# Optimization experiments

Hardware: AMD Instinct MI355X
Metric: run time of the kernel (lower is better)

## Reference

```python
import jax, jax.numpy as jnp
import numpy as np

D_MODEL = 1024
NUM_HEADS = 16
D_K = D_MODEL // NUM_HEADS
BATCH = 2
SEQ = 2048
SCALE = 1.0 / np.sqrt(D_K)


def _rope_tables(seq_len, d_k):
    # theta_i = 10000^(-2i/d_k), i in [0, d_k/2)
    theta = 10000.0 ** (-2.0 * jnp.arange(d_k // 2, dtype=jnp.float32) / d_k)
    angles = jnp.arange(seq_len, dtype=jnp.float32)[:, None] * theta[None, :]  # [S, d_k/2]
    return jnp.sin(angles), jnp.cos(angles)


def _apply_rope(x, sin, cos):
    # x: [B, H, S, d_k]; interleaved rotation over even/odd feature pairs
    xe = x[..., 0::2]
    xo = x[..., 1::2]
    re = xe * cos - xo * sin
    ro = xe * sin + xo * cos
    return jnp.stack([re, ro], axis=-1).reshape(x.shape)


def setup_inputs() -> dict:
    key = jax.random.key(0)
    ks = jax.random.split(key, 12)
    s = 0.02
    inp = {
        'q_input': jax.random.normal(ks[0], (BATCH, SEQ, D_MODEL), jnp.float32),
        'k_input': jax.random.normal(ks[1], (BATCH, SEQ, D_MODEL), jnp.float32),
        'v_input': jax.random.normal(ks[2], (BATCH, SEQ, D_MODEL), jnp.float32),
        'mask': jnp.tril(jnp.ones((SEQ, SEQ), jnp.int32)),  # causal 2D mask
        'W_q': jax.random.normal(ks[3], (D_MODEL, D_MODEL), jnp.float32) * s,
        'b_q': jnp.zeros((D_MODEL,), jnp.float32),
        'W_k': jax.random.normal(ks[4], (D_MODEL, D_MODEL), jnp.float32) * s,
        'b_k': jnp.zeros((D_MODEL,), jnp.float32),
        'W_v': jax.random.normal(ks[5], (D_MODEL, D_MODEL), jnp.float32) * s,
        'b_v': jnp.zeros((D_MODEL,), jnp.float32),
        'W_o': jax.random.normal(ks[6], (D_MODEL, D_MODEL), jnp.float32) * s,
        'b_o': jnp.zeros((D_MODEL,), jnp.float32),
    }
    return inp


def reference(q_input, k_input, v_input, mask, W_q, b_q, W_k, b_k, W_v, b_v, W_o, b_o):
    B, S, _ = q_input.shape
    # projections -> [B, H, S, d_k]
    def proj(x, W, b):
        y = x @ W + b
        return y.reshape(B, -1, NUM_HEADS, D_K).transpose(0, 2, 1, 3)
    q = proj(q_input, W_q, b_q)
    k = proj(k_input, W_k, b_k)
    v = proj(v_input, W_v, b_v)

    sin, cos = _rope_tables(S, D_K)
    q = _apply_rope(q, sin, cos)
    k = _apply_rope(k, sin, cos)

    scores = jnp.einsum('bhqd,bhkd->bhqk', q, k) * SCALE
    scores = jnp.where(mask[None, None, :, :] == 0, jnp.float32(-1e9), scores)
    attn = jax.nn.softmax(scores, axis=-1)  # dropout is identity (p=0 / eval)
    ctx = jnp.einsum('bhqk,bhkd->bhqd', attn, v)
    ctx = ctx.transpose(0, 2, 1, 3).reshape(B, S, D_MODEL)
    return ctx @ W_o + b_o
```

## Files before the change

kernel.cpp:

```cpp
#include <hip/hip_runtime.h>

typedef unsigned short u16;
typedef unsigned int u32;
typedef __attribute__((ext_vector_type(8))) short short8;
typedef __attribute__((ext_vector_type(4))) float f32x4;
typedef __attribute__((ext_vector_type(16))) float f32x16;

#define DEV static __device__ __forceinline__

DEV u16 f2bf(float x) {
  union { float f; u32 u; } v; v.f = x;
  u32 r = v.u + 0x7fffu + ((v.u >> 16) & 1u);
  return (u16)(r >> 16);
}
DEV float bf2f(u16 x) {
  union { u32 u; float f; } v; v.u = ((u32)x) << 16;
  return v.f;
}
DEV u32 cvtpk(float lo, float hi) {
  u32 r;
  asm("v_cvt_pk_bf16_f32 %0, %1, %2" : "=v"(r) : "v"(lo), "v"(hi));
  return r;
}
DEV void swap32(u32& a, u32& b) {
  asm("v_permlane32_swap_b32 %0, %1" : "+v"(a), "+v"(b));
}
DEV float ex2(float x) {
  float r;
  asm("v_exp_f32 %0, %1" : "=v"(r) : "v"(x));
  return r;
}

DEV void gload_lds16(const void* g, void* l) {
  __builtin_amdgcn_global_load_lds(
      (__attribute__((address_space(1))) u32*)((void*)g),
      (__attribute__((address_space(3))) u32*)l, 16, 0, 0);
}

DEV void mfma_bf16(f32x4& d, short8 a, short8 b) {
  asm("v_mfma_f32_16x16x32_bf16 %0, %1, %2, %0" : "+v"(d) : "v"(a), "v"(b));
}
DEV void mfma32(f32x16& d, short8 a, short8 b) {
  asm("v_mfma_f32_32x32x16_bf16 %0, %1, %2, %0" : "+v"(d) : "v"(a), "v"(b));
}

__global__ __launch_bounds__(256) void k_prep(const float* __restrict__ x0, const float* __restrict__ x1,
                                              const float* __restrict__ x2, u16* __restrict__ o0,
                                              u16* __restrict__ o1, u16* __restrict__ o2,
                                              const float* __restrict__ W0, const float* __restrict__ W1,
                                              const float* __restrict__ W2, const float* __restrict__ W3,
                                              u16* __restrict__ T0, u16* __restrict__ T1,
                                              u16* __restrict__ T2, u16* __restrict__ T3,
                                              float2* __restrict__ tab) {
  int bid = blockIdx.x;
  int t = threadIdx.x;
  if (bid < 6144) {
    int z = bid >> 11;
    const float* in = (z == 0) ? x0 : (z == 1) ? x1 : x2;
    u16* out = (z == 0) ? o0 : (z == 1) ? o1 : o2;
    int i = (bid & 2047) * 256 + t;
    const float4* p = (const float4*)in;
    float4 a = p[i * 2], b = p[i * 2 + 1];
    uint4 o;
    o.x = cvtpk(a.x, a.y); o.y = cvtpk(a.z, a.w);
    o.z = cvtpk(b.x, b.y); o.w = cvtpk(b.z, b.w);
    ((uint4*)out)[i] = o;
  } else if (bid < 7168) {
    int q = bid - 6144;
    int z = q >> 8;
    const float* W = (z == 0) ? W0 : (z == 1) ? W1 : (z == 2) ? W2 : W3;
    u16* Wt = (z == 0) ? T0 : (z == 1) ? T1 : (z == 2) ? T2 : T3;
    __shared__ u16 tile[64][65];
    int k0 = ((q >> 4) & 15) * 64, n0 = (q & 15) * 64;
    int rr = t >> 4, cc = (t & 15) * 4;
#pragma unroll
    for (int i = 0; i < 4; ++i) {
      int r = rr + i * 16;
      float4 v = *(const float4*)&W[(size_t)(k0 + r) * 1024 + n0 + cc];
      tile[r][cc + 0] = f2bf(v.x); tile[r][cc + 1] = f2bf(v.y);
      tile[r][cc + 2] = f2bf(v.z); tile[r][cc + 3] = f2bf(v.w);
    }
    __syncthreads();
#pragma unroll
    for (int i = 0; i < 4; ++i) {
      int n = rr + i * 16;
      u16 a0 = tile[cc + 0][n], a1 = tile[cc + 1][n], a2 = tile[cc + 2][n], a3 = tile[cc + 3][n];
      uint2 pk;
      pk.x = (u32)a0 | ((u32)a1 << 16);
      pk.y = (u32)a2 | ((u32)a3 << 16);
      *(uint2*)&Wt[(size_t)(n0 + n) * 1024 + k0 + cc] = pk;
    }
  } else {
    int idx = (bid - 7168) * 256 + t;
    int s = idx >> 5, dp = idx & 31;
    float theta = exp2f((float)dp * (-2.0f / 64.0f) * 13.287712379549449f);
    float ang = (float)s * theta;
    float sn, cs;
    sincosf(ang, &sn, &cs);
    tab[idx] = make_float2(cs, sn);
  }
}

#define GEMM_BODY(A_, Bt_)                                                                       \
  __shared__ __align__(16) char sA[16384];                                                       \
  __shared__ __align__(16) char sB[16384];                                                       \
  int tid = threadIdx.x, lane = tid & 63, w = tid >> 6;                                          \
  int l15 = lane & 15, lg = lane >> 4;                                                           \
  int bm = blockIdx.x * 128, bn = blockIdx.y * 128;                                              \
  int wm = (w >> 1) * 64, wn = (w & 1) * 64;                                                     \
  f32x4 acc[4][4];                                                                               \
  _Pragma("unroll") for (int i = 0; i < 4; ++i)                                                  \
      _Pragma("unroll") for (int j = 0; j < 4; ++j) acc[i][j] = (f32x4){0.f, 0.f, 0.f, 0.f};     \
  for (int kt = 0; kt < 16; ++kt) {                                                              \
    _Pragma("unroll") for (int p = 0; p < 4; ++p) {                                              \
      int idx = p * 256 + tid;                                                                   \
      int row = idx >> 3;                                                                        \
      int c8 = (idx & 7) ^ (row & 7);                                                            \
      gload_lds16(A_ + (size_t)(bm + row) * 1024 + kt * 64 + c8 * 8, sA + p * 4096 + w * 1024);  \
      gload_lds16(Bt_ + (size_t)(bn + row) * 1024 + kt * 64 + c8 * 8, sB + p * 4096 + w * 1024); \
    }                                                                                            \
    __syncthreads();                                                                             \
    short8 af[4][2], bf[4][2];                                                                   \
    _Pragma("unroll") for (int i = 0; i < 4; ++i) _Pragma("unroll") for (int s = 0; s < 2; ++s) { \
      int cs = ((s * 4 + lg) ^ (l15 & 7)) * 16;                                                  \
      af[i][s] = *(const short8*)(sA + (wm + i * 16 + l15) * 128 + cs);                          \
      bf[i][s] = *(const short8*)(sB + (wn + i * 16 + l15) * 128 + cs);                          \
    }                                                                                            \
    _Pragma("unroll") for (int s = 0; s < 2; ++s)                                                \
        _Pragma("unroll") for (int i = 0; i < 4; ++i)                                            \
            _Pragma("unroll") for (int j = 0; j < 4; ++j) mfma_bf16(acc[i][j], af[i][s], bf[j][s]); \
    __syncthreads();                                                                             \
  }

template <int MODE>
__global__ __launch_bounds__(256) void k_gemm(const u16* __restrict__ A, const u16* __restrict__ Bt,
                                              const float* __restrict__ bias, void* __restrict__ dst) {
  GEMM_BODY(A, Bt)
  float bv[4];
#pragma unroll
  for (int j = 0; j < 4; ++j) bv[j] = bias[bn + wn + j * 16 + l15];
#pragma unroll
  for (int i = 0; i < 4; ++i) {
#pragma unroll
    for (int j = 0; j < 4; ++j) {
#pragma unroll
      for (int r = 0; r < 4; ++r) {
        int m = bm + wm + i * 16 + lg * 4 + r;
        int n = bn + wn + j * 16 + l15;
        float v = acc[i][j][r] + bv[j];
        if (MODE == 0) {
          int bb = m >> 11, s = m & 2047, h = n >> 6, d = n & 63;
          ((u16*)dst)[(((size_t)(bb * 16 + h)) * 2048 + s) * 64 + d] = f2bf(v);
        } else {
          ((float*)dst)[(size_t)m * 1024 + n] = v;
        }
      }
    }
  }
}

__global__ __launch_bounds__(256) void k_gemm_qkv(const u16* __restrict__ Aq, const u16* __restrict__ Ak,
                                                  const u16* __restrict__ Av, const u16* __restrict__ Wq,
                                                  const u16* __restrict__ Wk, const u16* __restrict__ Wv,
                                                  const float* __restrict__ bq, const float* __restrict__ bk,
                                                  const float* __restrict__ bv,
                                                  const float2* __restrict__ tab, u16* __restrict__ Qo,
                                                  u16* __restrict__ Ko, u16* __restrict__ VTo) {
  int z = blockIdx.z;
  const u16* A = (z == 0) ? Aq : (z == 1) ? Ak : Av;
  const u16* Bt = (z == 0) ? Wq : (z == 1) ? Wk : Wv;
  const float* bias = (z == 0) ? bq : (z == 1) ? bk : bv;
  GEMM_BODY(A, Bt)
  float bvv[4];
#pragma unroll
  for (int j = 0; j < 4; ++j) bvv[j] = bias[bn + wn + j * 16 + l15];
  if (z == 2) {
#pragma unroll
    for (int i = 0; i < 4; ++i) {
#pragma unroll
      for (int j = 0; j < 4; ++j) {
        int m = bm + wm + i * 16 + lg * 4;
        int n = bn + wn + j * 16 + l15;
        int bb = m >> 11, s = m & 2047, h = n >> 6, d = n & 63;
        uint2 pk;
        pk.x = cvtpk(acc[i][j][0] + bvv[j], acc[i][j][1] + bvv[j]);
        pk.y = cvtpk(acc[i][j][2] + bvv[j], acc[i][j][3] + bvv[j]);
        *(uint2*)(VTo + (((size_t)(bb * 16 + h)) * 64 + d) * 2048 + s) = pk;
      }
    }
    return;
  }
  u16* dst = (z == 0) ? Qo : Ko;
  int odd = l15 & 1;
#pragma unroll
  for (int i = 0; i < 4; ++i) {
#pragma unroll
    for (int j = 0; j < 4; ++j) {
#pragma unroll
      for (int r = 0; r < 4; ++r) {
        int m = bm + wm + i * 16 + lg * 4 + r;
        int n = bn + wn + j * 16 + l15;
        float v = acc[i][j][r] + bvv[j];
        {
          int s = m & 2047;
          int dp = (j * 16 + l15) >> 1;
          float2 cs = tab[s * 32 + dp];
          float p = __shfl_xor(v, 1);
          float ps = p * cs.y;
          v = odd ? fmaf(v, cs.x, ps) : fmaf(v, cs.x, -ps);
        }
        int bb = m >> 11, ss = m & 2047, h = n >> 6, d = n & 63;
        dst[(((size_t)(bb * 16 + h)) * 2048 + ss) * 64 + d] = f2bf(v);
      }
    }
  }
}

__global__ __launch_bounds__(256, 1) void k_attn(const u16* __restrict__ Q, const u16* __restrict__ K,
                                                 const u16* __restrict__ Vt, u16* __restrict__ ctx) {
  __shared__ __align__(16) char sK[2][8192];
  __shared__ __align__(16) char sV[2][8192];
  const float KL2E = 0.18033688011112042f;
  int id = blockIdx.x;
  int bh = id & 31, pp = id >> 5;
  int tid = threadIdx.x;
  int w = tid >> 6, lane = tid & 63;
  int q31 = lane & 31, h = lane >> 5;
  const u16* Qg = Q + (size_t)bh * 131072;
  const u16* Kg = K + (size_t)bh * 131072;
  const u16* Vg = Vt + (size_t)bh * 131072;
  int bb = bh >> 4, hh = bh & 15;

#define STAGE(BUF, KV)                                                                         \
  {                                                                                            \
    _Pragma("unroll") for (int sp = 0; sp < 2; ++sp) {                                         \
      int idx = sp * 256 + tid;                                                                \
      int row = idx >> 3;                                                                      \
      int c16 = (idx & 7) ^ (row & 7);                                                         \
      gload_lds16(Kg + (size_t)((KV) + row) * 64 + c16 * 8, sK[BUF] + sp * 4096 + w * 1024);   \
      gload_lds16(Vg + (size_t)row * 2048 + (KV) + c16 * 8, sV[BUF] + sp * 4096 + w * 1024);   \
    }                                                                                          \
  }

  for (int pass = 0; pass < 2; ++pass) {
    int qt = pass ? (15 - pp) : pp;
    int qbase = qt * 128 + w * 32;
    int qrow = qbase + q31;
    int ntile = 2 * qt + 2;
    STAGE(0, 0);
    short8 qf[4];
#pragma unroll
    for (int m = 0; m < 4; ++m)
      qf[m] = *(const short8*)(Qg + (size_t)qrow * 64 + m * 16 + h * 8);
    f32x16 o0, o1;
#pragma unroll
    for (int r = 0; r < 16; ++r) { o0[r] = 0.f; o1[r] = 0.f; }
    float mrun = -3e38f, lrun = 0.f;
    __syncthreads();

    for (int t = 0; t < ntile; ++t) {
      int kv = t << 6, cur = t & 1;
      if (t + 1 < ntile) STAGE(cur ^ 1, (t + 1) << 6);
      if (kv <= qbase + 31) {
        char* sKc = sK[cur];
        char* sVc = sV[cur];
        int swz = (q31 & 7) << 4;
        short8 kf0[4], kf1[4];
#pragma unroll
        for (int m = 0; m < 4; ++m) {
          int cb = (2 * m + h) * 16;
          kf0[m] = *(const short8*)(sKc + q31 * 128 + (cb ^ swz));
          kf1[m] = *(const short8*)(sKc + (32 + q31) * 128 + (cb ^ swz));
        }
        f32x16 pA, pB;
#pragma unroll
        for (int r = 0; r < 16; ++r) { pA[r] = 0.f; pB[r] = 0.f; }
#pragma unroll
        for (int m = 0; m < 4; ++m) mfma32(pA, kf0[m], qf[m]);
#pragma unroll
        for (int m = 0; m < 4; ++m) mfma32(pB, kf1[m], qf[m]);

        if (kv + 63 > qbase) {
#pragma unroll
          for (int r = 0; r < 16; ++r) {
            int keyA = kv + (r & 3) + 8 * (r >> 2) + 4 * h;
            if (keyA > qrow) pA[r] = -1e9f;
            if (keyA + 32 > qrow) pB[r] = -1e9f;
          }
        }
        float pm = pA[0];
#pragma unroll
        for (int r = 1; r < 16; ++r) pm = fmaxf(pm, pA[r]);
#pragma unroll
        for (int r = 0; r < 16; ++r) pm = fmaxf(pm, pB[r]);
        pm = fmaxf(pm, __shfl_xor(pm, 32));
        float mnew = fmaxf(mrun, pm);
        int upd = pm > mrun;
        float alpha = ex2((mrun - mnew) * KL2E);
        mrun = mnew;
        float ps = 0.f;
#pragma unroll
        for (int r = 0; r < 16; ++r) {
          pA[r] = ex2((pA[r] - mnew) * KL2E);
          ps += pA[r];
        }
#pragma unroll
        for (int r = 0; r < 16; ++r) {
          pB[r] = ex2((pB[r] - mnew) * KL2E);
          ps += pB[r];
        }
        ps += __shfl_xor(ps, 32);
        lrun = lrun * alpha + ps;
        if (__any(upd)) {
#pragma unroll
          for (int r = 0; r < 16; ++r) { o0[r] *= alpha; o1[r] *= alpha; }
        }
        short8 vf0[4], vf1[4];
#pragma unroll
        for (int m = 0; m < 4; ++m) {
          int cb = (2 * m + h) * 16;
          vf0[m] = *(const short8*)(sVc + q31 * 128 + (cb ^ swz));
          vf1[m] = *(const short8*)(sVc + (32 + q31) * 128 + (cb ^ swz));
        }
#pragma unroll
        for (int m = 0; m < 4; ++m) {
          int mlow = 8 * (m & 1);
          u32 u0, u1, v0, v1;
          if (m < 2) {
            u0 = cvtpk(pA[mlow + 0], pA[mlow + 1]);
            u1 = cvtpk(pA[mlow + 2], pA[mlow + 3]);
            v0 = cvtpk(pA[mlow + 4], pA[mlow + 5]);
            v1 = cvtpk(pA[mlow + 6], pA[mlow + 7]);
          } else {
            u0 = cvtpk(pB[mlow + 0], pB[mlow + 1]);
            u1 = cvtpk(pB[mlow + 2], pB[mlow + 3]);
            v0 = cvtpk(pB[mlow + 4], pB[mlow + 5]);
            v1 = cvtpk(pB[mlow + 6], pB[mlow + 7]);
          }
          swap32(u0, v0);
          swap32(u1, v1);
          union { u32 wd[4]; short8 s; } pf;
          pf.wd[0] = u0; pf.wd[1] = u1; pf.wd[2] = v0; pf.wd[3] = v1;
          mfma32(o0, vf0[m], pf.s);
          mfma32(o1, vf1[m], pf.s);
        }
      }
      __syncthreads();
    }

    float rl = 1.f / lrun;
    u16* base = ctx + ((size_t)(bb * 2048 + qrow)) * 1024 + hh * 64;
#pragma unroll
    for (int r = 0; r < 4; ++r) {
      uint2 pk;
      pk.x = cvtpk(o0[4 * r + 0] * rl, o0[4 * r + 1] * rl);
      pk.y = cvtpk(o0[4 * r + 2] * rl, o0[4 * r + 3] * rl);
      *(uint2*)(base + 8 * r + 4 * h) = pk;
      uint2 pk2;
      pk2.x = cvtpk(o1[4 * r + 0] * rl, o1[4 * r + 1] * rl);
      pk2.y = cvtpk(o1[4 * r + 2] * rl, o1[4 * r + 3] * rl);
      *(uint2*)(base + 32 + 8 * r + 4 * h) = pk2;
    }
  }
#undef STAGE
}

extern "C" void kernel_launch(void* const* d_in, const int* in_sizes, int n_in,
                              void* d_out, int out_size, void* d_ws, size_t ws_size,
                              hipStream_t stream) {
  (void)in_sizes; (void)n_in; (void)out_size; (void)ws_size;
  const float* xq = (const float*)d_in[0];
  const float* xk = (const float*)d_in[1];
  const float* xv = (const float*)d_in[2];
  const float* Wq = (const float*)d_in[4];
  const float* bq = (const float*)d_in[5];
  const float* Wk = (const float*)d_in[6];
  const float* bk = (const float*)d_in[7];
  const float* Wv = (const float*)d_in[8];
  const float* bv = (const float*)d_in[9];
  const float* Wo = (const float*)d_in[10];
  const float* bo = (const float*)d_in[11];

  char* ws = (char*)d_ws;
  u16* XQ  = (u16*)(ws);
  u16* XK  = (u16*)(ws + ((size_t)8 << 20));
  u16* XV  = (u16*)(ws + ((size_t)16 << 20));
  u16* WTQ = (u16*)(ws + ((size_t)24 << 20));
  u16* WTK = (u16*)(ws + ((size_t)26 << 20));
  u16* WTV = (u16*)(ws + ((size_t)28 << 20));
  u16* WTO = (u16*)(ws + ((size_t)30 << 20));
  u16* Qb  = (u16*)(ws + ((size_t)32 << 20));
  u16* Kb  = (u16*)(ws + ((size_t)40 << 20));
  u16* VT  = (u16*)(ws + ((size_t)48 << 20));
  u16* CTX = (u16*)(ws);
  float2* TAB = (float2*)d_out;

  k_prep<<<7424, 256, 0, stream>>>(xq, xk, xv, XQ, XK, XV, Wq, Wk, Wv, Wo, WTQ, WTK, WTV, WTO, TAB);
  dim3 gq(32, 8, 3);
  k_gemm_qkv<<<gq, 256, 0, stream>>>(XQ, XK, XV, WTQ, WTK, WTV, bq, bk, bv, TAB, Qb, Kb, VT);
  k_attn<<<256, 256, 0, stream>>>(Qb, Kb, VT, CTX);
  dim3 gg(32, 8);
  k_gemm<1><<<gg, 256, 0, stream>>>(CTX, WTO, bo, d_out);
}
```

Baseline: 120.4 us.

## Widen attention KV tile from 64 to 128 keys with wider V swizzle

Each inner iteration of the attention kernel now processes 128 keys instead of 64. The K and V LDS buffers are doubled and the V tile uses a 16-chunk XOR swizzle over 256-byte rows. This halves the number of barriers and softmax rescale steps per query tile, and the max and sum reductions become tree-shaped to shorten dependency chains. The cost is more register pressure from four score accumulators, twice the LDS use, and wasted masked work in the diagonal tile, since per-warp skipping of fully masked subtiles is gone.

Result: faster. 115.7 us (-4.0%).

```diff
diff --git a/kernel.cpp b/kernel.cpp
--- a/kernel.cpp
+++ b/kernel.cpp
@@ -218,8 +218,8 @@
 
 __global__ __launch_bounds__(256, 1) void k_attn(const u16* __restrict__ Q, const u16* __restrict__ K,
                                                  const u16* __restrict__ Vt, u16* __restrict__ ctx) {
-  __shared__ __align__(16) char sK[2][8192];
-  __shared__ __align__(16) char sV[2][8192];
+  __shared__ __align__(16) char sK[2][16384];
+  __shared__ __align__(16) char sV[2][16384];
   const float KL2E = 0.18033688011112042f;
   int id = blockIdx.x;
   int bh = id & 31, pp = id >> 5;
@@ -231,22 +231,24 @@
   const u16* Vg = Vt + (size_t)bh * 131072;
   int bb = bh >> 4, hh = bh & 15;
 
-#define STAGE(BUF, KV)                                                                         \
-  {                                                                                            \
-    _Pragma("unroll") for (int sp = 0; sp < 2; ++sp) {                                         \
-      int idx = sp * 256 + tid;                                                                \
-      int row = idx >> 3;                                                                      \
-      int c16 = (idx & 7) ^ (row & 7);                                                         \
-      gload_lds16(Kg + (size_t)((KV) + row) * 64 + c16 * 8, sK[BUF] + sp * 4096 + w * 1024);   \
-      gload_lds16(Vg + (size_t)row * 2048 + (KV) + c16 * 8, sV[BUF] + sp * 4096 + w * 1024);   \
-    }                                                                                          \
+#define STAGE(BUF, KV)                                                                          \
+  {                                                                                             \
+    _Pragma("unroll") for (int sp = 0; sp < 4; ++sp) {                                          \
+      int idx = sp * 256 + tid;                                                                 \
+      int krow = idx >> 3;                                                                      \
+      int kc = (idx & 7) ^ (krow & 7);                                                          \
+      gload_lds16(Kg + (size_t)((KV) + krow) * 64 + kc * 8, sK[BUF] + sp * 4096 + w * 1024);    \
+      int vrow = idx >> 4;                                                                      \
+      int vc = (idx & 15) ^ (vrow & 15);                                                        \
+      gload_lds16(Vg + (size_t)vrow * 2048 + (KV) + vc * 8, sV[BUF] + sp * 4096 + w * 1024);    \
+    }                                                                                           \
   }
 
   for (int pass = 0; pass < 2; ++pass) {
     int qt = pass ? (15 - pp) : pp;
     int qbase = qt * 128 + w * 32;
     int qrow = qbase + q31;
-    int ntile = 2 * qt + 2;
+    int ntile = qt + 1;
     STAGE(0, 0);
     short8 qf[4];
 #pragma unroll
@@ -259,91 +261,93 @@
     __syncthreads();
 
     for (int t = 0; t < ntile; ++t) {
-      int kv = t << 6, cur = t & 1;
-      if (t + 1 < ntile) STAGE(cur ^ 1, (t + 1) << 6);
-      if (kv <= qbase + 31) {
-        char* sKc = sK[cur];
-        char* sVc = sV[cur];
-        int swz = (q31 & 7) << 4;
-        short8 kf0[4], kf1[4];
-#pragma unroll
-        for (int m = 0; m < 4; ++m) {
-          int cb = (2 * m + h) * 16;
-          kf0[m] = *(const short8*)(sKc + q31 * 128 + (cb ^ swz));
-          kf1[m] = *(const short8*)(sKc + (32 + q31) * 128 + (cb ^ swz));
+      int kv = t << 7, cur = t & 1;
+      if (t + 1 < ntile) STAGE(cur ^ 1, (t + 1) << 7);
+      char* sKc = sK[cur];
+      char* sVc = sV[cur];
+      int swzk = (q31 & 7) << 4;
+      f32x16 p0, p1, p2, p3;
+#pragma unroll
+      for (int r = 0; r < 16; ++r) { p0[r] = 0.f; p1[r] = 0.f; p2[r] = 0.f; p3[r] = 0.f; }
+#define QKF(PF, F)                                                                              \
+  {                                                                                             \
+    _Pragma("unroll") for (int m = 0; m < 4; ++m) {                                             \
+      short8 kf = *(const short8*)(sKc + ((F) * 32 + q31) * 128 + (((2 * m + h) << 4) ^ swzk)); \
+      mfma32(PF, kf, qf[m]);                                                                    \
+    }                                                                                           \
+  }
+      QKF(p0, 0) QKF(p1, 1) QKF(p2, 2) QKF(p3, 3)
+#undef QKF
+
+      if (t == ntile - 1) {
+#pragma unroll
+        for (int r = 0; r < 16; ++r) {
+          int keyb = kv + (r & 3) + 8 * (r >> 2) + 4 * h;
+          if (keyb > qrow) p0[r] = -1e9f;
+          if (keyb + 32 > qrow) p1[r] = -1e9f;
+          if (keyb + 64 > qrow) p2[r] = -1e9f;
+          if (keyb + 96 > qrow) p3[r] = -1e9f;
         }
-        f32x16 pA, pB;
-#pragma unroll
-        for (int r = 0; r < 16; ++r) { pA[r] = 0.f; pB[r] = 0.f; }
-#pragma unroll
-        for (int m = 0; m < 4; ++m) mfma32(pA, kf0[m], qf[m]);
-#pragma unroll
-        for (int m = 0; m < 4; ++m) mfma32(pB, kf1[m], qf[m]);
-
-        if (kv + 63 > qbase) {
-#pragma unroll
-          for (int r = 0; r < 16; ++r) {
-            int keyA = kv + (r & 3) + 8 * (r >> 2) + 4 * h;
-            if (keyA > qrow) pA[r] = -1e9f;
-            if (keyA + 32 > qrow) pB[r] = -1e9f;
-          }
+      }
+      float t16[16];
+#pragma unroll
+      for (int r = 0; r < 16; ++r)
+        t16[r] = fmaxf(fmaxf(p0[r], p1[r]), fmaxf(p2[r], p3[r]));
+#pragma unroll
+      for (int s = 8; s >= 1; s >>= 1)
+#pragma unroll
+        for (int r = 0; r < 8; ++r)
+          if (r < s) t16[r] = fmaxf(t16[r], t16[r + s]);
+      float pm = t16[0];
+      pm = fmaxf(pm, __shfl_xor(pm, 32));
+      float mnew = fmaxf(mrun, pm);
+      int upd = pm > mrun;
+      float alpha = ex2((mrun - mnew) * KL2E);
+      mrun = mnew;
+      float sacc[8];
+#pragma unroll
+      for (int i = 0; i < 8; ++i) sacc[i] = 0.f;
+#pragma unroll
+      for (int r = 0; r < 16; ++r) { p0[r] = ex2((p0[r] - mnew) * KL2E); sacc[r & 7] += p0[r]; }
+#pragma unroll
+      for (int r = 0; r < 16; ++r) { p1[r] = ex2((p1[r] - mnew) * KL2E); sacc[r & 7] += p1[r]; }
+#pragma unroll
+      for (int r = 0; r < 16; ++r) { p2[r] = ex2((p2[r] - mnew) * KL2E); sacc[r & 7] += p2[r]; }
+#pragma unroll
+      for (int r = 0; r < 16; ++r) { p3[r] = ex2((p3[r] - mnew) * KL2E); sacc[r & 7] += p3[r]; }
+      float ps = ((sacc[0] + sacc[1]) + (sacc[2] + sacc[3])) + ((sacc[4] + sacc[5]) + (sacc[6] + sacc[7]));
+      ps += __shfl_xor(ps, 32);
+      lrun = lrun * alpha + ps;
+      if (__any(upd)) {
+#pragma unroll
+        for (int r = 0; r < 16; ++r) { o0[r] *= alpha; o1[r] *= alpha; }
+      }
+#pragma unroll
+      for (int m = 0; m < 8; ++m) {
+        int mlow = 8 * (m & 1);
+        u32 u0, u1, v0, v1;
+        if (m < 2) {
+          u0 = cvtpk(p0[mlow + 0], p0[mlow + 1]); u1 = cvtpk(p0[mlow + 2], p0[mlow + 3]);
+          v0 = cvtpk(p0[mlow + 4], p0[mlow + 5]); v1 = cvtpk(p0[mlow + 6], p0[mlow + 7]);
+        } else if (m < 4) {
+          u0 = cvtpk(p1[mlow + 0], p1[mlow + 1]); u1 = cvtpk(p1[mlow + 2], p1[mlow + 3]);
+          v0 = cvtpk(p1[mlow + 4], p1[mlow + 5]); v1 = cvtpk(p1[mlow + 6], p1[mlow + 7]);
+        } else if (m < 6) {
+          u0 = cvtpk(p2[mlow + 0], p2[mlow + 1]); u1 = cvtpk(p2[mlow + 2], p2[mlow + 3]);
+          v0 = cvtpk(p2[mlow + 4], p2[mlow + 5]); v1 = cvtpk(p2[mlow + 6], p2[mlow + 7]);
+        } else {
+          u0 = cvtpk(p3[mlow + 0], p3[mlow + 1]); u1 = cvtpk(p3[mlow + 2], p3[mlow + 3]);
+          v0 = cvtpk(p3[mlow + 4], p3[mlow + 5]); v1 = cvtpk(p3[mlow + 6], p3[mlow + 7]);
         }
-        float pm = pA[0];
-#pragma unroll
-        for (int r = 1; r < 16; ++r) pm = fmaxf(pm, pA[r]);
-#pragma unroll
-        for (int r = 0; r < 16; ++r) pm = fmaxf(pm, pB[r]);
-        pm = fmaxf(pm, __shfl_xor(pm, 32));
-        float mnew = fmaxf(mrun, pm);
-        int upd = pm > mrun;
-        float alpha = ex2((mrun - mnew) * KL2E);
-        mrun = mnew;
-        float ps = 0.f;
-#pragma unroll
-        for (int r = 0; r < 16; ++r) {
-          pA[r] = ex2((pA[r] - mnew) * KL2E);
-          ps += pA[r];
-        }
-#pragma unroll
-        for (int r = 0; r < 16; ++r) {
-          pB[r] = ex2((pB[r] - mnew) * KL2E);
-          ps += pB[r];
-        }
-        ps += __shfl_xor(ps, 32);
-        lrun = lrun * alpha + ps;
-        if (__any(upd)) {
-#pragma unroll
-          for (int r = 0; r < 16; ++r) { o0[r] *= alpha; o1[r] *= alpha; }
-        }
-        short8 vf0[4], vf1[4];
-#pragma unroll
-        for (int m = 0; m < 4; ++m) {
-          int cb = (2 * m + h) * 16;
-          vf0[m] = *(const short8*)(sVc + q31 * 128 + (cb ^ swz));
-          vf1[m] = *(const short8*)(sVc + (32 + q31) * 128 + (cb ^ swz));
-        }
-#pragma unroll
-        for (int m = 0; m < 4; ++m) {
-          int mlow = 8 * (m & 1);
-          u32 u0, u1, v0, v1;
-          if (m < 2) {
-            u0 = cvtpk(pA[mlow + 0], pA[mlow + 1]);
-            u1 = cvtpk(pA[mlow + 2], pA[mlow + 3]);
-            v0 = cvtpk(pA[mlow + 4], pA[mlow + 5]);
-            v1 = cvtpk(pA[mlow + 6], pA[mlow + 7]);
-          } else {
-            u0 = cvtpk(pB[mlow + 0], pB[mlow + 1]);
-            u1 = cvtpk(pB[mlow + 2], pB[mlow + 3]);
-            v0 = cvtpk(pB[mlow + 4], pB[mlow + 5]);
-            v1 = cvtpk(pB[mlow + 6], pB[mlow + 7]);
-          }
-          swap32(u0, v0);
-          swap32(u1, v1);
-          union { u32 wd[4]; short8 s; } pf;
-          pf.wd[0] = u0; pf.wd[1] = u1; pf.wd[2] = v0; pf.wd[3] = v1;
-          mfma32(o0, vf0[m], pf.s);
-          mfma32(o1, vf1[m], pf.s);
-        }
+        swap32(u0, v0);
+        swap32(u1, v1);
+        union { u32 wd[4]; short8 s; } pf;
+        pf.wd[0] = u0; pf.wd[1] = u1; pf.wd[2] = v0; pf.wd[3] = v1;
+        int vcol = ((2 * m + h) ^ (q31 & 15)) << 4;
+        short8 vf0 = *(const short8*)(sVc + q31 * 256 + vcol);
+        short8 vf1 = *(const short8*)(sVc + (32 + q31) * 256 + vcol);
+        mfma32(o0, vf0, pf.s);
+        mfma32(o1, vf1, pf.s);
       }
       __syncthreads();
     }
```
